# Kernel tuning notes

Measured on AMD Instinct MI355X. Metric: run time of the kernel, lower is better.

The kernel has to match this reference:

```python
import math
import jax, jax.numpy as jnp
import numpy as np

NUM_HEADS = 40
HEAD_DIM = 128
HIDDEN = NUM_HEADS * HEAD_DIM  # 5120
BATCH = 1
SEQ = 2048


def _alibi_slopes(n: int):
    """Standard ALiBi slopes (handles non-power-of-2 head counts)."""
    def pow2_slopes(k):
        start = 2.0 ** (-(2.0 ** -(math.log2(k) - 3)))
        return [start * (start ** i) for i in range(k)]
    if math.log2(n).is_integer():
        return pow2_slopes(n)
    closest = 2 ** int(math.floor(math.log2(n)))
    return pow2_slopes(closest) + _alibi_slopes(2 * closest)[0::2][: n - closest]


def setup_inputs() -> dict:
    key = jax.random.key(0)
    k1, k2, k3 = jax.random.split(key, 3)
    hidden_states = jax.random.normal(k1, (BATCH, SEQ, HIDDEN), dtype=jnp.float32)
    # fused QKV weight, no bias (Baichuan W_pack)
    w_pack = jax.random.normal(k2, (3 * HIDDEN, HIDDEN), dtype=jnp.float32) * (HIDDEN ** -0.5)
    w_o = jax.random.normal(k3, (HIDDEN, HIDDEN), dtype=jnp.float32) * (HIDDEN ** -0.5)
    return {"hidden_states": hidden_states, "w_pack": w_pack, "w_o": w_o}


def reference(hidden_states, w_pack, w_o):
    B, S, H = hidden_states.shape
    nh, hd = NUM_HEADS, HEAD_DIM

    # fused QKV projection, then chunk(3, -1)
    qkv = jnp.einsum('bsh,oh->bso', hidden_states, w_pack)  # [B,S,3H]
    q, k, v = jnp.split(qkv, 3, axis=-1)
    q = q.reshape(B, S, nh, hd).transpose(0, 2, 1, 3)  # [B,nh,S,hd]
    k = k.reshape(B, S, nh, hd).transpose(0, 2, 1, 3)
    v = v.reshape(B, S, nh, hd).transpose(0, 2, 1, 3)

    scale = 1.0 / math.sqrt(hd)
    scores = jnp.einsum('bhqd,bhkd->bhqk', q, k) * scale  # [B,nh,S,S]

    # ALiBi bias: -slope * (q_pos - k_pos) for k_pos <= q_pos
    slopes = jnp.asarray(_alibi_slopes(nh), dtype=scores.dtype)  # [nh]
    pos = jnp.arange(S)
    rel = (pos[:, None] - pos[None, :]).astype(scores.dtype)  # [S,S] q - k
    bias = -slopes[:, None, None] * rel  # [nh,S,S]
    causal = pos[:, None] >= pos[None, :]
    neg_inf = jnp.asarray(jnp.finfo(scores.dtype).min, scores.dtype)
    scores = jnp.where(causal[None, None], scores + bias[None], neg_inf)

    attn = jax.nn.softmax(scores, axis=-1)
    out = jnp.einsum('bhqk,bhkd->bhqd', attn, v)  # [B,nh,S,hd]
    out = out.transpose(0, 2, 1, 3).reshape(B, S, H)
    return jnp.einsum('bsh,oh->bso', out, w_o)  # o_proj, no bias
```

## Files before the change

kernel.cpp:

```cpp
#include <hip/hip_runtime.h>
#include <hip/hip_bf16.h>
#include <cstdint>


typedef __attribute__((ext_vector_type(8))) short  bf16x8_t;
typedef __attribute__((ext_vector_type(4))) float  f32x4_t;

#define S_LEN   2048
#define HIDDEN  5120
#define NHEADS  40
#define HDIM    128
#define QKV_N   15360
#define LOG2E   1.44269504088896f

__device__ __forceinline__ unsigned short f2bf(float x) {
  unsigned u = __builtin_bit_cast(unsigned, x);
  u += 0x7fffu + ((u >> 16) & 1u);
  return (unsigned short)(u >> 16);
}

__device__ __forceinline__ void gll16(const void* g, void* l) {
  __builtin_amdgcn_global_load_lds(
      (const __attribute__((address_space(1))) unsigned int*)g,
      (__attribute__((address_space(3))) unsigned int*)l, 16, 0, 0);
}

__global__ void __launch_bounds__(256)
cast_f32_bf16(const float* __restrict__ in, unsigned short* __restrict__ out,
              const int n8) {
  const int i = blockIdx.x * 256 + threadIdx.x;
  if (i >= n8) return;
  const f32x4_t a = ((const f32x4_t*)in)[2 * i];
  const f32x4_t b = ((const f32x4_t*)in)[2 * i + 1];
  bf16x8_t o;
#pragma unroll
  for (int j = 0; j < 4; ++j) {
    o[j]     = (short)f2bf(a[j]);
    o[4 + j] = (short)f2bf(b[j]);
  }
  ((bf16x8_t*)out)[i] = o;
}

template <typename OutT>
__global__ void __launch_bounds__(256, 2)
gemm_bt(const unsigned short* __restrict__ A, const unsigned short* __restrict__ B,
        OutT* __restrict__ C, const int M, const int N, const int K) {
  __shared__ unsigned short lA[128 * 32];
  __shared__ unsigned short lB[128 * 32];

  const int tid = threadIdx.x;
  const int wid = tid >> 6, lane = tid & 63;

  int wg = blockIdx.x;
  {
    const int nwg = gridDim.x;
    if ((nwg & 7) == 0) { const int cpx = nwg >> 3; wg = (wg & 7) * cpx + (wg >> 3); }
  }
  const int nbn = N >> 7;
  const int bi = wg / nbn, bj = wg % nbn;
  const int wr = wid >> 1, wc = wid & 1;
  const size_t sK = (size_t)K;

  const int arow = wid * 16 + (lane >> 2);
  const int acol = (lane & 3) * 8;
  const unsigned short* gA0 = A + (size_t)(bi * 128 + arow) * sK + acol;
  const unsigned short* gB0 = B + (size_t)(bj * 128 + arow) * sK + acol;
  unsigned short* lA0 = &lA[wid * 16 * 32];
  unsigned short* lB0 = &lB[wid * 16 * 32];

  f32x4_t acc[4][4];
#pragma unroll
  for (int m = 0; m < 4; ++m)
#pragma unroll
    for (int n = 0; n < 4; ++n) acc[m][n] = (f32x4_t){0.f, 0.f, 0.f, 0.f};

  const int rs = (lane & 15) * 32 + (lane >> 4) * 8;

  for (int k0 = 0; k0 < K; k0 += 32) {
    gll16(gA0 + k0,           lA0);
    gll16(gA0 + 64 * sK + k0, lA0 + 64 * 32);
    gll16(gB0 + k0,           lB0);
    gll16(gB0 + 64 * sK + k0, lB0 + 64 * 32);
    __syncthreads();

    bf16x8_t a[4], b[4];
#pragma unroll
    for (int m = 0; m < 4; ++m) a[m] = *(const bf16x8_t*)&lA[(wr * 64 + m * 16) * 32 + rs];
#pragma unroll
    for (int n = 0; n < 4; ++n) b[n] = *(const bf16x8_t*)&lB[(wc * 64 + n * 16) * 32 + rs];
#pragma unroll
    for (int m = 0; m < 4; ++m)
#pragma unroll
      for (int n = 0; n < 4; ++n)
        acc[m][n] = __builtin_amdgcn_mfma_f32_16x16x32_bf16(a[m], b[n], acc[m][n], 0, 0, 0);
    __syncthreads();
  }

  const int r0 = bi * 128 + wr * 64 + (lane >> 4) * 4;
  const int c0 = bj * 128 + wc * 64 + (lane & 15);
#pragma unroll
  for (int m = 0; m < 4; ++m)
#pragma unroll
    for (int n = 0; n < 4; ++n)
#pragma unroll
      for (int r = 0; r < 4; ++r) {
        const size_t idx = (size_t)(r0 + m * 16 + r) * N + (c0 + n * 16);
        if constexpr (sizeof(OutT) == 2) C[idx] = (OutT)f2bf(acc[m][n][r]);
        else                             C[idx] = acc[m][n][r];
      }
}

__global__ void __launch_bounds__(256, 2)
attn_kernel(const unsigned short* __restrict__ qkv, unsigned short* __restrict__ ao) {
  __shared__ unsigned short Kl[64 * 128];
  __shared__ unsigned short Vt[128 * 64];
  __shared__ unsigned short Pl[128 * 64];

  const int tid = threadIdx.x;
  const int wid = tid >> 6, lane = tid & 63;
  const int g = lane >> 4, li = lane & 15;
  const int qb = blockIdx.x;
  const int h  = blockIdx.y;

  const float slope = (h < 32) ? exp2f(-0.25f * (float)(h + 1))
                               : exp2f(-0.125f * (float)(2 * (h - 32) + 1));
  const float scale = 0.08838834764831845f;

  const unsigned short* Qg = qkv + (size_t)h * HDIM;
  const unsigned short* Kg = qkv + HIDDEN + (size_t)h * HDIM;
  const unsigned short* Vg = qkv + 2 * HIDDEN + (size_t)h * HDIM;

  const int q0 = qb * 128 + wid * 32;

  bf16x8_t qf[2][4];
#pragma unroll
  for (int m = 0; m < 2; ++m)
#pragma unroll
    for (int ds = 0; ds < 4; ++ds)
      qf[m][ds] = *(const bf16x8_t*)&Qg[(size_t)(q0 + m * 16 + li) * QKV_N + ds * 32 + g * 8];

  f32x4_t o_acc[2][8];
  float m_run[2][4], l_run[2][4];
#pragma unroll
  for (int m = 0; m < 2; ++m) {
#pragma unroll
    for (int nn = 0; nn < 8; ++nn) o_acc[m][nn] = (f32x4_t){0.f, 0.f, 0.f, 0.f};
#pragma unroll
    for (int r = 0; r < 4; ++r) { m_run[m][r] = -INFINITY; l_run[m][r] = 0.f; }
  }

  const int ntiles = 2 * qb + 2;
  for (int t = 0; t < ntiles; ++t) {
    const int kt = t * 64;
    __syncthreads();

#pragma unroll
    for (int c = 0; c < 4; ++c) {
      const int rowbase = c * 16 + wid * 4;
      const int row = rowbase + g;
      const int col = (li * 8) ^ ((row & 7) << 3);
      gll16(&Kg[(size_t)(kt + row) * QKV_N + col], &Kl[rowbase * 128]);
    }
#pragma unroll
    for (int c = 0; c < 4; ++c) {
      const int e = c * 256 + tid;
      const int d = e & 127;
      const int k0 = (e >> 7) * 8;
      bf16x8_t pk;
#pragma unroll
      for (int j = 0; j < 8; ++j)
        pk[j] = (short)Vg[(size_t)(kt + k0 + j) * QKV_N + d];
      *(bf16x8_t*)((char*)Vt + (((d * 64 + k0) * 2) ^ ((d & 7) << 4))) = pk;
    }
    __syncthreads();

    f32x4_t sacc[2][4];
#pragma unroll
    for (int m = 0; m < 2; ++m)
#pragma unroll
      for (int n = 0; n < 4; ++n) sacc[m][n] = (f32x4_t){0.f, 0.f, 0.f, 0.f};
#pragma unroll
    for (int ds = 0; ds < 4; ++ds) {
#pragma unroll
      for (int n = 0; n < 4; ++n) {
        const int row = n * 16 + li;
        const bf16x8_t kf = *(const bf16x8_t*)((const char*)Kl +
            (((row * 128 + ds * 32 + g * 8) * 2) ^ ((row & 7) << 4)));
#pragma unroll
        for (int m = 0; m < 2; ++m)
          sacc[m][n] = __builtin_amdgcn_mfma_f32_16x16x32_bf16(qf[m][ds], kf, sacc[m][n], 0, 0, 0);
      }
    }

    float corr[2][4];
#pragma unroll
    for (int m = 0; m < 2; ++m) {
#pragma unroll
      for (int r = 0; r < 4; ++r) {
        const int qg = q0 + m * 16 + g * 4 + r;
        float s[4];
#pragma unroll
        for (int n = 0; n < 4; ++n) {
          const int kg = kt + n * 16 + li;
          const float v = sacc[m][n][r] * scale - slope * (float)(qg - kg);
          s[n] = (kg <= qg) ? v : -INFINITY;
        }
        float mx = fmaxf(fmaxf(s[0], s[1]), fmaxf(s[2], s[3]));
#pragma unroll
        for (int off = 1; off < 16; off <<= 1) mx = fmaxf(mx, __shfl_xor(mx, off));
        const float mnew = fmaxf(m_run[m][r], mx);
        float p[4], psum = 0.f;
#pragma unroll
        for (int n = 0; n < 4; ++n) { p[n] = exp2f((s[n] - mnew) * LOG2E); psum += p[n]; }
#pragma unroll
        for (int off = 1; off < 16; off <<= 1) psum += __shfl_xor(psum, off);
        const float cr = exp2f((m_run[m][r] - mnew) * LOG2E);
        corr[m][r] = cr;
        l_run[m][r] = l_run[m][r] * cr + psum;
        m_run[m][r] = mnew;
        const int q = wid * 32 + m * 16 + g * 4 + r;
#pragma unroll
        for (int n = 0; n < 4; ++n) {
          const int kc = n * 16 + li;
          Pl[(q * 64 + kc) ^ ((q & 7) << 3)] = f2bf(p[n]);
        }
      }
    }
#pragma unroll
    for (int m = 0; m < 2; ++m)
#pragma unroll
      for (int nn = 0; nn < 8; ++nn)
#pragma unroll
        for (int r = 0; r < 4; ++r) o_acc[m][nn][r] *= corr[m][r];

#pragma unroll
    for (int ks = 0; ks < 2; ++ks) {
      bf16x8_t pf[2];
#pragma unroll
      for (int m = 0; m < 2; ++m) {
        const int q = wid * 32 + m * 16 + li;
        pf[m] = *(const bf16x8_t*)((const char*)Pl +
            (((q * 64 + ks * 32 + g * 8) * 2) ^ ((q & 7) << 4)));
      }
#pragma unroll
      for (int nn = 0; nn < 8; ++nn) {
        const int d = nn * 16 + li;
        const bf16x8_t vf = *(const bf16x8_t*)((const char*)Vt +
            (((d * 64 + ks * 32 + g * 8) * 2) ^ ((d & 7) << 4)));
#pragma unroll
        for (int m = 0; m < 2; ++m)
          o_acc[m][nn] = __builtin_amdgcn_mfma_f32_16x16x32_bf16(pf[m], vf, o_acc[m][nn], 0, 0, 0);
      }
    }
  }

#pragma unroll
  for (int m = 0; m < 2; ++m)
#pragma unroll
    for (int r = 0; r < 4; ++r) {
      const float inv = 1.0f / l_run[m][r];
      const int qg = q0 + m * 16 + g * 4 + r;
#pragma unroll
      for (int nn = 0; nn < 8; ++nn) {
        const int d = nn * 16 + li;
        ao[(size_t)qg * HIDDEN + h * HDIM + d] = f2bf(o_acc[m][nn][r] * inv);
      }
    }
}

extern "C" void kernel_launch(void* const* d_in, const int* in_sizes, int n_in,
                              void* d_out, int out_size, void* d_ws, size_t ws_size,
                              hipStream_t stream) {
  const float* hs = (const float*)d_in[0];
  const float* wp = (const float*)d_in[1];
  const float* wo = (const float*)d_in[2];
  float* out = (float*)d_out;

  char* ws = (char*)d_ws;
  unsigned short* wpb = (unsigned short*)(ws);
  unsigned short* hsb = (unsigned short*)(ws + 157286400);
  unsigned short* qkv = (unsigned short*)(ws + 178257920);
  unsigned short* ao  = (unsigned short*)(ws + 241172480);
  unsigned short* wob = (unsigned short*)(ws);

  cast_f32_bf16<<<38400, 256, 0, stream>>>(wp, wpb, 9830400);
  cast_f32_bf16<<<5120, 256, 0, stream>>>(hs, hsb, 1310720);

  gemm_bt<unsigned short><<<16 * 120, 256, 0, stream>>>(hsb, wpb, qkv, S_LEN, QKV_N, HIDDEN);

  cast_f32_bf16<<<12800, 256, 0, stream>>>(wo, wob, 3276800);

  attn_kernel<<<dim3(16, NHEADS), 256, 0, stream>>>(qkv, ao);

  gemm_bt<float><<<16 * 40, 256, 0, stream>>>(ao, wob, out, S_LEN, HIDDEN, HIDDEN);
}
```

Before: 1.601 ms.

## Split causal attention over KV chunks, pre-transpose V, double-buffer K/V

Replaces the one-block-per-query-tile attention with a split-KV scheme of 1600 balanced work items (up to 512 keys each), followed by a combine kernel that merges partial outputs using saved max and sum statistics. V is pre-transposed into a scratch buffer so it can be staged with async global-to-LDS loads, and K/V tiles are double-buffered so the next tile's loads overlap the current tile's compute. The aim is to fix load imbalance and low occupancy in causal attention and to remove the strided scalar V gather. The cost is extra fp32 partial-output traffic, two extra kernel launches, and reuse of the output buffer as scratch for transposed V.

```diff
diff --git a/kernel.cpp b/kernel.cpp
--- a/kernel.cpp
+++ b/kernel.cpp
@@ -110,17 +110,51 @@
       }
 }
 
+__global__ void __launch_bounds__(256)
+transpose_v(const unsigned short* __restrict__ qkv, unsigned short* __restrict__ vT) {
+  __shared__ unsigned short t[64][72];
+  const int s0 = blockIdx.x * 64;
+  const int d0 = blockIdx.y * 64;
+  const int r = threadIdx.x >> 3, c8 = (threadIdx.x & 7) * 8;
+#pragma unroll
+  for (int rr = 0; rr < 64; rr += 32) {
+    bf16x8_t v = *(const bf16x8_t*)&qkv[(size_t)(s0 + r + rr) * QKV_N + 2 * HIDDEN + d0 + c8];
+    *(bf16x8_t*)&t[r + rr][c8] = v;
+  }
+  __syncthreads();
+#pragma unroll
+  for (int rr = 0; rr < 64; rr += 32) {
+    const int dd = r + rr;
+    bf16x8_t o;
+#pragma unroll
+    for (int j = 0; j < 8; ++j) o[j] = (short)t[c8 + j][dd];
+    *(bf16x8_t*)&vT[(size_t)(d0 + dd) * S_LEN + s0 + c8] = o;
+  }
+}
+
 __global__ void __launch_bounds__(256, 2)
-attn_kernel(const unsigned short* __restrict__ qkv, unsigned short* __restrict__ ao) {
-  __shared__ unsigned short Kl[64 * 128];
-  __shared__ unsigned short Vt[128 * 64];
+attn_split(const unsigned short* __restrict__ qkv, const unsigned short* __restrict__ vT,
+           float* __restrict__ Opart, float* __restrict__ Ml) {
+  __shared__ unsigned short Kl[2][64 * 128];
+  __shared__ unsigned short Vt[2][128 * 64];
   __shared__ unsigned short Pl[128 * 64];
 
   const int tid = threadIdx.x;
   const int wid = tid >> 6, lane = tid & 63;
   const int g = lane >> 4, li = lane & 15;
-  const int qb = blockIdx.x;
-  const int h  = blockIdx.y;
+
+  int slot = blockIdx.x;
+  { const int cpx = 1600 >> 3; slot = (slot & 7) * cpx + (slot >> 3); }
+  const int h = slot / 40, rr_ = slot % 40;
+  int qt, kc;
+  if      (rr_ < 4)  { qt = rr_;                 kc = 0; }
+  else if (rr_ < 12) { qt = 4 + ((rr_ - 4) >> 1);  kc = (rr_ - 4) & 1; }
+  else if (rr_ < 24) { qt = 8 + (rr_ - 12) / 3;    kc = (rr_ - 12) % 3; }
+  else               { qt = 12 + ((rr_ - 24) >> 2); kc = (rr_ - 24) & 3; }
+  const int kvs = kc * 512;
+  const int kvend_full = (qt + 1) * 128;
+  const int kvend = (kvend_full < kvs + 512) ? kvend_full : (kvs + 512);
+  const int ntiles = (kvend - kvs) >> 6;
 
   const float slope = (h < 32) ? exp2f(-0.25f * (float)(h + 1))
                                : exp2f(-0.125f * (float)(2 * (h - 32) + 1));
@@ -128,9 +162,9 @@
 
   const unsigned short* Qg = qkv + (size_t)h * HDIM;
   const unsigned short* Kg = qkv + HIDDEN + (size_t)h * HDIM;
-  const unsigned short* Vg = qkv + 2 * HIDDEN + (size_t)h * HDIM;
-
-  const int q0 = qb * 128 + wid * 32;
+  const unsigned short* Vh = vT + (size_t)h * HDIM * S_LEN;
+
+  const int q0 = qt * 128 + wid * 32;
 
   bf16x8_t qf[2][4];
 #pragma unroll
@@ -149,30 +183,33 @@
     for (int r = 0; r < 4; ++r) { m_run[m][r] = -INFINITY; l_run[m][r] = 0.f; }
   }
 
-  const int ntiles = 2 * qb + 2;
-  for (int t = 0; t < ntiles; ++t) {
-    const int kt = t * 64;
-    __syncthreads();
-
+  auto stageK = [&](int buf, int t) {
 #pragma unroll
     for (int c = 0; c < 4; ++c) {
       const int rowbase = c * 16 + wid * 4;
       const int row = rowbase + g;
       const int col = (li * 8) ^ ((row & 7) << 3);
-      gll16(&Kg[(size_t)(kt + row) * QKV_N + col], &Kl[rowbase * 128]);
-    }
+      gll16(&Kg[(size_t)(kvs + t * 64 + row) * QKV_N + col], &Kl[buf][rowbase * 128]);
+    }
+  };
+  auto stageV = [&](int buf, int t) {
 #pragma unroll
     for (int c = 0; c < 4; ++c) {
-      const int e = c * 256 + tid;
-      const int d = e & 127;
-      const int k0 = (e >> 7) * 8;
-      bf16x8_t pk;
-#pragma unroll
-      for (int j = 0; j < 8; ++j)
-        pk[j] = (short)Vg[(size_t)(kt + k0 + j) * QKV_N + d];
-      *(bf16x8_t*)((char*)Vt + (((d * 64 + k0) * 2) ^ ((d & 7) << 4))) = pk;
-    }
-    __syncthreads();
+      const int rowbase = c * 32 + wid * 8;
+      const int row = rowbase + (lane >> 3);
+      const int col = ((lane & 7) ^ (row & 7)) * 8;
+      gll16(&Vh[(size_t)row * S_LEN + kvs + t * 64 + col], &Vt[buf][rowbase * 64]);
+    }
+  };
+
+  stageK(0, 0);
+  stageV(0, 0);
+  __syncthreads();
+
+  for (int t = 0; t < ntiles; ++t) {
+    const int cur = t & 1;
+    if (t + 1 < ntiles) { stageK(cur ^ 1, t + 1); stageV(cur ^ 1, t + 1); }
+    const int kt = kvs + t * 64;
 
     f32x4_t sacc[2][4];
 #pragma unroll
@@ -184,7 +221,7 @@
 #pragma unroll
       for (int n = 0; n < 4; ++n) {
         const int row = n * 16 + li;
-        const bf16x8_t kf = *(const bf16x8_t*)((const char*)Kl +
+        const bf16x8_t kf = *(const bf16x8_t*)((const char*)&Kl[cur][0] +
             (((row * 128 + ds * 32 + g * 8) * 2) ^ ((row & 7) << 4)));
 #pragma unroll
         for (int m = 0; m < 2; ++m)
@@ -221,8 +258,8 @@
         const int q = wid * 32 + m * 16 + g * 4 + r;
 #pragma unroll
         for (int n = 0; n < 4; ++n) {
-          const int kc = n * 16 + li;
-          Pl[(q * 64 + kc) ^ ((q & 7) << 3)] = f2bf(p[n]);
+          const int kcl = n * 16 + li;
+          Pl[(q * 64 + kcl) ^ ((q & 7) << 3)] = f2bf(p[n]);
         }
       }
     }
@@ -245,27 +282,77 @@
 #pragma unroll
       for (int nn = 0; nn < 8; ++nn) {
         const int d = nn * 16 + li;
-        const bf16x8_t vf = *(const bf16x8_t*)((const char*)Vt +
+        const bf16x8_t vf = *(const bf16x8_t*)((const char*)&Vt[cur][0] +
             (((d * 64 + ks * 32 + g * 8) * 2) ^ ((d & 7) << 4)));
 #pragma unroll
         for (int m = 0; m < 2; ++m)
           o_acc[m][nn] = __builtin_amdgcn_mfma_f32_16x16x32_bf16(pf[m], vf, o_acc[m][nn], 0, 0, 0);
       }
     }
-  }
-
+    __syncthreads();
+  }
+
+  const int slotbase = slot;
 #pragma unroll
   for (int m = 0; m < 2; ++m)
 #pragma unroll
     for (int r = 0; r < 4; ++r) {
-      const float inv = 1.0f / l_run[m][r];
-      const int qg = q0 + m * 16 + g * 4 + r;
+      const int row = wid * 32 + m * 16 + g * 4 + r;
+      if (li == 0) {
+        Ml[(size_t)slotbase * 256 + row * 2 + 0] = m_run[m][r];
+        Ml[(size_t)slotbase * 256 + row * 2 + 1] = l_run[m][r];
+      }
 #pragma unroll
       for (int nn = 0; nn < 8; ++nn) {
         const int d = nn * 16 + li;
-        ao[(size_t)qg * HIDDEN + h * HDIM + d] = f2bf(o_acc[m][nn][r] * inv);
-      }
-    }
+        Opart[(size_t)slotbase * 16384 + row * 128 + d] = o_acc[m][nn][r];
+      }
+    }
+}
+
+__global__ void __launch_bounds__(256)
+combine_kernel(const float* __restrict__ Opart, const float* __restrict__ Ml,
+               unsigned short* __restrict__ ao) {
+  const int b = blockIdx.x;
+  const int h = b >> 4, qt = b & 15;
+  const int nc = (qt >> 2) + 1;
+  const int base = (qt < 4) ? qt : (qt < 8) ? 4 + 2 * (qt - 4)
+                 : (qt < 12) ? 12 + 3 * (qt - 8) : 24 + 4 * (qt - 12);
+  const int slot0 = h * 40 + base;
+  const int row = threadIdx.x >> 1, d0 = (threadIdx.x & 1) * 64;
+
+  float mi[4], li_[4];
+  float M = -INFINITY;
+#pragma unroll
+  for (int i = 0; i < 4; ++i) {
+    if (i < nc) {
+      mi[i]  = Ml[(size_t)(slot0 + i) * 256 + row * 2 + 0];
+      li_[i] = Ml[(size_t)(slot0 + i) * 256 + row * 2 + 1];
+      M = fmaxf(M, mi[i]);
+    }
+  }
+  float w[4], L = 0.f;
+#pragma unroll
+  for (int i = 0; i < 4; ++i) {
+    w[i] = (i < nc) ? exp2f((mi[i] - M) * LOG2E) : 0.f;
+    if (i < nc) L += w[i] * li_[i];
+  }
+  const float inv = 1.0f / L;
+  const size_t orow = (size_t)(qt * 128 + row) * HIDDEN + h * HDIM;
+
+  for (int dd = d0; dd < d0 + 64; dd += 4) {
+    f32x4_t acc = (f32x4_t){0.f, 0.f, 0.f, 0.f};
+#pragma unroll
+    for (int i = 0; i < 4; ++i) {
+      if (i < nc) {
+        const f32x4_t o = *(const f32x4_t*)&Opart[(size_t)(slot0 + i) * 16384 + row * 128 + dd];
+#pragma unroll
+        for (int j = 0; j < 4; ++j) acc[j] += w[i] * o[j];
+      }
+    }
+#pragma unroll
+    for (int j = 0; j < 4; ++j) ao[orow + dd + j] = f2bf(acc[j] * inv);
+  }
 }
 
 extern "C" void kernel_launch(void* const* d_in, const int* in_sizes, int n_in,
@@ -282,15 +369,22 @@
   unsigned short* qkv = (unsigned short*)(ws + 178257920);
   unsigned short* ao  = (unsigned short*)(ws + 241172480);
   unsigned short* wob = (unsigned short*)(ws);
+  float* Opart = (float*)(ws + 52428800);
+  float* Ml    = (float*)(ws + 157286400);
+  unsigned short* vTb = (unsigned short*)d_out;
 
   cast_f32_bf16<<<38400, 256, 0, stream>>>(wp, wpb, 9830400);
   cast_f32_bf16<<<5120, 256, 0, stream>>>(hs, hsb, 1310720);
 
-  gemm_bt<unsigned short><<<16 * 120, 256, 0, stream>>>(hsb, wpb, qkv, S_LEN, QKV_N, HIDDEN);
+  gemm_bt<unsigned short><<<1920, 256, 0, stream>>>(hsb, wpb, qkv, S_LEN, QKV_N, HIDDEN);
 
   cast_f32_bf16<<<12800, 256, 0, stream>>>(wo, wob, 3276800);
 
-  attn_kernel<<<dim3(16, NHEADS), 256, 0, stream>>>(qkv, ao);
-
-  gemm_bt<float><<<16 * 40, 256, 0, stream>>>(ao, wob, out, S_LEN, HIDDEN, HIDDEN);
-}
+  transpose_v<<<dim3(32, 80), 256, 0, stream>>>(qkv, vTb);
+
+  attn_split<<<1600, 256, 0, stream>>>(qkv, vTb, Opart, Ml);
+
+  combine_kernel<<<640, 256, 0, stream>>>(Opart, Ml, ao);
+
+  gemm_bt<float><<<640, 256, 0, stream>>>(ao, wob, out, S_LEN, HIDDEN, HIDDEN);
+}
```

New measurement: 1.525 ms. 4.8% less time.
